# Kernel optimization log

Hardware: AMD Instinct MI355X
Metric: run time of the kernel (lower is better)

The kernel has to match this reference:

```python
import jax, jax.numpy as jnp
import numpy as np

EMBED_DIM = 1024
NUM_HEADS = 16
HEAD_DIM = EMBED_DIM // NUM_HEADS


def setup_inputs() -> dict:
    key = jax.random.key(0)
    ks = jax.random.split(key, 7)
    B, S, E = 2, 2048, EMBED_DIM
    s = 1.0 / np.sqrt(E)
    return {
        "x": jax.random.normal(ks[0], (B, S, E), dtype=jnp.float32),
        "W_qkv": jax.random.uniform(ks[1], (3 * E, E), jnp.float32, -s, s),
        "b_qkv": jax.random.uniform(ks[2], (3 * E,), jnp.float32, -s, s),
        "W_proj": jax.random.uniform(ks[3], (E, E), jnp.float32, -s, s),
        "b_proj": jax.random.uniform(ks[4], (E,), jnp.float32, -s, s),
        "gamma": jnp.ones((E,), jnp.float32),
        "beta": jnp.zeros((E,), jnp.float32),
    }


def reference(x, W_qkv, b_qkv, W_proj, b_proj, gamma, beta):
    B, S, E = x.shape
    H, D = NUM_HEADS, HEAD_DIM
    residual = x
    # fused QKV projection: [B,S,3E] -> [B,S,3,H,D]
    qkv = (jnp.einsum('bse,fe->bsf', x, W_qkv) + b_qkv).reshape(B, S, 3, H, D)
    q = qkv[:, :, 0].transpose(0, 2, 1, 3)  # [B,H,S,D]
    k = qkv[:, :, 1].transpose(0, 2, 1, 3)
    v = qkv[:, :, 2].transpose(0, 2, 1, 3)
    scale = 1.0 / jnp.sqrt(jnp.float32(D)).astype(x.dtype)
    attn = jnp.einsum('bhqd,bhkd->bhqk', q, k) * scale  # [B,H,S,S]
    attn = jax.nn.softmax(attn, axis=-1)
    out = jnp.einsum('bhqk,bhkd->bhqd', attn, v)  # [B,H,S,D]
    out = out.transpose(0, 2, 1, 3).reshape(B, S, E)
    out = jnp.einsum('bse,fe->bsf', out, W_proj) + b_proj
    # LayerNorm(out + residual), eps=1e-5 (torch default)
    y = out + residual
    mu = jnp.mean(y, axis=-1, keepdims=True)
    var = jnp.mean(jnp.square(y - mu), axis=-1, keepdims=True)
    return (y - mu) * jax.lax.rsqrt(var + 1e-5) * gamma + beta
```

## Files before the change

### kernel.cpp

```cpp
#include <hip/hip_runtime.h>
#include <cstdint>

#define EDIM 1024
#define NHEADS 16
#define HDIM 64
#define BATCH 2
#define SEQ 2048
#define MROWS (BATCH * SEQ)

typedef __attribute__((ext_vector_type(8))) short bf16x8;
typedef __attribute__((ext_vector_type(4))) float f32x4;

#define QSCALE 0.18033688011112042f

__device__ __forceinline__ unsigned short f2bf(float f) {
  union { float f; unsigned u; } v; v.f = f;
  unsigned r = v.u + 0x7FFFu + ((v.u >> 16) & 1u);
  return (unsigned short)(r >> 16);
}

__device__ __forceinline__ unsigned cvt_pk_bf16(float lo, float hi) {
  unsigned r;
  asm("v_cvt_pk_bf16_f32 %0, %1, %2" : "=v"(r) : "v"(lo), "v"(hi));
  return r;
}

__device__ __forceinline__ void gload16(const void* g, void* l) {
  __builtin_amdgcn_global_load_lds(
      (const __attribute__((address_space(1))) unsigned int*)g,
      (__attribute__((address_space(3))) unsigned int*)l, 16, 0, 0);
}

__global__ __launch_bounds__(256) void cvt_all_kernel(
    const float* __restrict__ x, const float* __restrict__ wq,
    const float* __restrict__ wp, unsigned short* __restrict__ xo,
    unsigned short* __restrict__ wqo, unsigned short* __restrict__ wpo) {
  const int NX = MROWS * EDIM, NQ = 3 * EDIM * EDIM, NP = EDIM * EDIM;
  int i = (blockIdx.x * 256 + threadIdx.x) * 8;
  const float* src;
  unsigned short* dst;
  if (i < NX) {
    src = x + i; dst = xo + i;
  } else if (i < NX + NQ) {
    src = wq + (i - NX); dst = wqo + (i - NX);
  } else if (i < NX + NQ + NP) {
    src = wp + (i - NX - NQ); dst = wpo + (i - NX - NQ);
  } else {
    return;
  }
  const float4 a = *(const float4*)&src[0];
  const float4 b = *(const float4*)&src[4];
  unsigned u[4];
  u[0] = cvt_pk_bf16(a.x, a.y);
  u[1] = cvt_pk_bf16(a.z, a.w);
  u[2] = cvt_pk_bf16(b.x, b.y);
  u[3] = cvt_pk_bf16(b.z, b.w);
  *(uint4*)dst = *(uint4*)u;
}

template <int MODE>
__global__ __launch_bounds__(256) void gemm_bf16(
    const unsigned short* __restrict__ A, const unsigned short* __restrict__ Bw,
    const float* __restrict__ bias, const float* __restrict__ resid,
    unsigned short* __restrict__ q_out, unsigned short* __restrict__ k_out,
    unsigned short* __restrict__ v_out, float* __restrict__ y_out,
    int M, int N, int K) {
  __shared__ unsigned short As[128 * 64];
  __shared__ unsigned short Bs[128 * 64];
  const int tid = threadIdx.x;
  const int lane = tid & 63, w = tid >> 6;
  const int wr = w >> 1, wc = w & 1;
  const int l15 = lane & 15, g = lane >> 4;

  const int flat = blockIdx.y * gridDim.x + blockIdx.x;
  const int xk = flat & 7, xi = flat >> 3;
  int bx, by;
  if (MODE == 0) { bx = xk * 3 + (xi >> 5); by = xi & 31; }
  else           { bx = xk;                 by = xi; }
  const int row0 = by * 128, col0 = bx * 128;

  const int er = w * 32 + (lane >> 3);
  const int ec = (lane & 7) * 8;

  f32x4 acc[4][4];
#pragma unroll
  for (int i = 0; i < 4; ++i)
#pragma unroll
    for (int j = 0; j < 4; ++j) acc[i][j] = (f32x4){0.f, 0.f, 0.f, 0.f};

  for (int k0 = 0; k0 < K; k0 += 64) {
    __syncthreads();
#pragma unroll
    for (int t = 0; t < 4; ++t) {
      gload16(&A[(size_t)(row0 + er + t * 8) * K + k0 + ec],
              &As[w * 2048 + t * 512]);
      gload16(&Bw[(size_t)(col0 + er + t * 8) * K + k0 + ec],
              &Bs[w * 2048 + t * 512]);
    }
    __syncthreads();
#pragma unroll
    for (int ks = 0; ks < 2; ++ks) {
      bf16x8 af[4], bfr[4];
#pragma unroll
      for (int i = 0; i < 4; ++i)
        af[i] = *(const bf16x8*)&As[(wr * 64 + i * 16 + l15) * 64 + ks * 32 + g * 8];
#pragma unroll
      for (int j = 0; j < 4; ++j)
        bfr[j] = *(const bf16x8*)&Bs[(wc * 64 + j * 16 + l15) * 64 + ks * 32 + g * 8];
#pragma unroll
      for (int i = 0; i < 4; ++i)
#pragma unroll
        for (int j = 0; j < 4; ++j)
          acc[i][j] = __builtin_amdgcn_mfma_f32_16x16x32_bf16(af[i], bfr[j],
                                                              acc[i][j], 0, 0, 0);
    }
  }

#pragma unroll
  for (int j = 0; j < 4; ++j) {
    const int nbase = col0 + wc * 64 + j * 16 + l15;
    const float bb = bias[nbase];
#pragma unroll
    for (int i = 0; i < 4; ++i) {
#pragma unroll
      for (int r = 0; r < 4; ++r) {
        const int m = row0 + wr * 64 + i * 16 + g * 4 + r;
        float v = acc[i][j][r] + bb;
        if (MODE == 0) {
          const int which = nbase >> 10;
          const int h = (nbase >> 6) & 15, d = nbase & 63;
          const int b = m >> 11, s = m & 2047;
          const size_t idx = ((size_t)(b * NHEADS + h) * SEQ + s) * HDIM + d;
          if (which == 0) q_out[idx] = f2bf(v * QSCALE);
          else if (which == 1) k_out[idx] = f2bf(v);
          else v_out[idx] = f2bf(v);
        } else {
          v += resid[(size_t)m * N + nbase];
          y_out[(size_t)m * N + nbase] = v;
        }
      }
    }
  }
}

__global__ __launch_bounds__(256) void vtrans_kernel(
    const unsigned short* __restrict__ V, unsigned short* __restrict__ Vt) {
  __shared__ unsigned short T[64 * 72];
  const int tid = threadIdx.x;
  const int st = blockIdx.x, bh = blockIdx.y;
  const size_t ibase = (size_t)bh * SEQ * HDIM + (size_t)st * 64 * HDIM;
#pragma unroll
  for (int t = 0; t < 2; ++t) {
    const int chunk = t * 256 + tid;
    const int r = chunk >> 3, c8 = chunk & 7;
    const uint4 v = *(const uint4*)&V[ibase + r * 64 + c8 * 8];
    *(uint4*)&T[r * 72 + c8 * 8] = v;
  }
  __syncthreads();
  const size_t obase = (size_t)bh * HDIM * SEQ + st * 64;
#pragma unroll
  for (int t = 0; t < 2; ++t) {
    const int chunk = t * 256 + tid;
    const int d = chunk >> 3, s8 = (chunk & 7) * 8;
    unsigned short u[8];
#pragma unroll
    for (int e = 0; e < 8; ++e) u[e] = T[(s8 + e) * 72 + d];
    *(uint4*)&Vt[obase + (size_t)d * SEQ + s8] = *(uint4*)u;
  }
}

__global__ __launch_bounds__(512, 4) void attn_mfma(
    const unsigned short* __restrict__ Qb, const unsigned short* __restrict__ Kb,
    const unsigned short* __restrict__ Vt, unsigned short* __restrict__ AO) {
  __shared__ unsigned short K_lds[2][64 * 64];
  __shared__ unsigned short V_lds[2][64 * 64];
  __shared__ unsigned P32[128 * 32];
  const int tid = threadIdx.x;
  const int lane = tid & 63, w = tid >> 6;
  const int l15 = lane & 15, g = lane >> 4;
  const int qt = blockIdx.x;
  const int bh = blockIdx.y;
  const int b = bh >> 4, h = bh & 15;
  const size_t hbase = (size_t)bh * SEQ * HDIM;
  const size_t vbase = (size_t)bh * HDIM * SEQ;
  const int q = qt * 128 + w * 16 + l15;
  const int prow32 = (w * 16 + l15) * 32;

  const int sr = (w & 3) * 16 + (lane >> 3);
  const int scol = ((lane & 7) ^ (lane >> 3)) * 8;

  bf16x8 aq[2];
#pragma unroll
  for (int ks = 0; ks < 2; ++ks)
    aq[ks] = *(const bf16x8*)&Qb[hbase + (size_t)q * HDIM + ks * 32 + g * 8];

  f32x4 o[4];
#pragma unroll
  for (int jd = 0; jd < 4; ++jd) o[jd] = (f32x4){0.f, 0.f, 0.f, 0.f};
  float mi = -1e30f, li = 0.f;

#define STAGE(buf, kt_)                                                        \
  do {                                                                         \
    if (w < 4) {                                                               \
      gload16(&Kb[hbase + (size_t)((kt_) * 64 + sr) * HDIM + scol],            \
              &K_lds[buf][(w * 16) * 64]);                                     \
      gload16(&Kb[hbase + (size_t)((kt_) * 64 + sr + 8) * HDIM + scol],        \
              &K_lds[buf][(w * 16 + 8) * 64]);                                 \
    } else {                                                                   \
      gload16(&Vt[vbase + (size_t)sr * SEQ + (kt_) * 64 + scol],               \
              &V_lds[buf][((w - 4) * 16) * 64]);                               \
      gload16(&Vt[vbase + (size_t)(sr + 8) * SEQ + (kt_) * 64 + scol],         \
              &V_lds[buf][((w - 4) * 16 + 8) * 64]);                           \
    }                                                                          \
  } while (0)

  STAGE(0, 0);
  for (int kt = 0; kt < SEQ / 64; ++kt) {
    const int cur = kt & 1;
    __syncthreads();
    if (kt + 1 < SEQ / 64) STAGE(cur ^ 1, kt + 1);

    f32x4 scT[4];
#pragma unroll
    for (int j = 0; j < 4; ++j) scT[j] = (f32x4){0.f, 0.f, 0.f, 0.f};
    __builtin_amdgcn_s_setprio(1);
#pragma unroll
    for (int ks = 0; ks < 2; ++ks) {
      bf16x8 bk[4];
#pragma unroll
      for (int j = 0; j < 4; ++j)
        bk[j] = *(const bf16x8*)&K_lds[cur][(j * 16 + l15) * 64 +
                                            (((ks * 4 + g) ^ (l15 & 7)) * 8)];
#pragma unroll
      for (int j = 0; j < 4; ++j)
        scT[j] = __builtin_amdgcn_mfma_f32_16x16x32_bf16(bk[j], aq[ks],
                                                         scT[j], 0, 0, 0);
    }
    __builtin_amdgcn_s_setprio(0);

    float tm = scT[0][0];
#pragma unroll
    for (int j = 0; j < 4; ++j)
#pragma unroll
      for (int r = 0; r < 4; ++r) tm = fmaxf(tm, scT[j][r]);
    tm = fmaxf(tm, __shfl_xor(tm, 16));
    tm = fmaxf(tm, __shfl_xor(tm, 32));
    const bool defer = __all(tm <= mi + 8.f) != 0;
    float al = 1.f;
    if (!defer) {
      const float mn = fmaxf(mi, tm);
      al = exp2f(mi - mn);
      mi = mn;
#pragma unroll
      for (int jd = 0; jd < 4; ++jd)
#pragma unroll
        for (int r = 0; r < 4; ++r) o[jd][r] *= al;
    }
    float p[4][4];
    float rs = 0.f;
#pragma unroll
    for (int j = 0; j < 4; ++j)
#pragma unroll
      for (int r = 0; r < 4; ++r) {
        p[j][r] = exp2f(scT[j][r] - mi);
        rs += p[j][r];
      }
    rs += __shfl_xor(rs, 16);
    rs += __shfl_xor(rs, 32);
    li = li * al + rs;

#pragma unroll
    for (int j = 0; j < 4; ++j) {
      const unsigned u01 = cvt_pk_bf16(p[j][0], p[j][1]);
      const unsigned u23 = cvt_pk_bf16(p[j][2], p[j][3]);
      const int c = (j * 4 + g) ^ l15;
      *(uint2*)&P32[prow32 + c * 2] = make_uint2(u01, u23);
    }

    __builtin_amdgcn_s_setprio(1);
#pragma unroll
    for (int ks = 0; ks < 2; ++ks) {
      const int cb = ks * 8 + g * 2;
      const uint2 a0 = *(const uint2*)&P32[prow32 + ((cb) ^ l15) * 2];
      const uint2 a1 = *(const uint2*)&P32[prow32 + ((cb + 1) ^ l15) * 2];
      unsigned pa[4] = {a0.x, a0.y, a1.x, a1.y};
      const bf16x8 ap = *(const bf16x8*)pa;
      bf16x8 bv[4];
#pragma unroll
      for (int jd = 0; jd < 4; ++jd)
        bv[jd] = *(const bf16x8*)&V_lds[cur][(jd * 16 + l15) * 64 +
                                             (((ks * 4 + g) ^ (l15 & 7)) * 8)];
#pragma unroll
      for (int jd = 0; jd < 4; ++jd)
        o[jd] = __builtin_amdgcn_mfma_f32_16x16x32_bf16(bv[jd], ap, o[jd], 0, 0, 0);
    }
    __builtin_amdgcn_s_setprio(0);
  }
#undef STAGE

  const float inv = 1.f / li;
#pragma unroll
  for (int jd = 0; jd < 4; ++jd) {
    uint2 u;
    u.x = cvt_pk_bf16(o[jd][0] * inv, o[jd][1] * inv);
    u.y = cvt_pk_bf16(o[jd][2] * inv, o[jd][3] * inv);
    *(uint2*)&AO[(size_t)(b * SEQ + q) * EDIM + h * HDIM + jd * 16 + g * 4] = u;
  }
}

__global__ __launch_bounds__(256) void ln_kernel(float* __restrict__ y,
                                                 const float* __restrict__ gamma,
                                                 const float* __restrict__ beta) {
  const int row = blockIdx.x, tid = threadIdx.x;
  const float4 v = *reinterpret_cast<const float4*>(&y[(size_t)row * EDIM + tid * 4]);
  float s = v.x + v.y + v.z + v.w;
  float s2 = v.x * v.x + v.y * v.y + v.z * v.z + v.w * v.w;
#pragma unroll
  for (int off = 1; off < 64; off <<= 1) {
    s += __shfl_xor(s, off);
    s2 += __shfl_xor(s2, off);
  }
  __shared__ float red[8];
  if ((tid & 63) == 0) {
    red[(tid >> 6) * 2 + 0] = s;
    red[(tid >> 6) * 2 + 1] = s2;
  }
  __syncthreads();
  s = red[0] + red[2] + red[4] + red[6];
  s2 = red[1] + red[3] + red[5] + red[7];
  const float mean = s * (1.f / 1024.f);
  const float var = fmaxf(s2 * (1.f / 1024.f) - mean * mean, 0.f);
  const float rstd = rsqrtf(var + 1e-5f);
  const float4 gm = *reinterpret_cast<const float4*>(&gamma[tid * 4]);
  const float4 be = *reinterpret_cast<const float4*>(&beta[tid * 4]);
  float4 outv;
  outv.x = (v.x - mean) * rstd * gm.x + be.x;
  outv.y = (v.y - mean) * rstd * gm.y + be.y;
  outv.z = (v.z - mean) * rstd * gm.z + be.z;
  outv.w = (v.w - mean) * rstd * gm.w + be.w;
  *reinterpret_cast<float4*>(&y[(size_t)row * EDIM + tid * 4]) = outv;
}

extern "C" void kernel_launch(void* const* d_in, const int* in_sizes, int n_in,
                              void* d_out, int out_size, void* d_ws,
                              size_t ws_size, hipStream_t stream) {
  const float* x = (const float*)d_in[0];
  const float* W_qkv = (const float*)d_in[1];
  const float* b_qkv = (const float*)d_in[2];
  const float* W_proj = (const float*)d_in[3];
  const float* b_proj = (const float*)d_in[4];
  const float* gamma = (const float*)d_in[5];
  const float* beta = (const float*)d_in[6];
  float* out = (float*)d_out;

  uint8_t* p = (uint8_t*)d_ws;
  unsigned short* x_bf = (unsigned short*)p;            p += (size_t)MROWS * EDIM * 2;
  unsigned short* wqkv_bf = (unsigned short*)p;         p += (size_t)3 * EDIM * EDIM * 2;
  unsigned short* wproj_bf = (unsigned short*)p;        p += (size_t)EDIM * EDIM * 2;
  unsigned short* Qb = (unsigned short*)p;              p += (size_t)MROWS * EDIM * 2;
  unsigned short* Kb = (unsigned short*)p;              p += (size_t)MROWS * EDIM * 2;
  unsigned short* Vb = (unsigned short*)p;              p += (size_t)MROWS * EDIM * 2;
  unsigned short* Vtb = (unsigned short*)p;             p += (size_t)MROWS * EDIM * 2;
  unsigned short* AOb = (unsigned short*)p;             p += (size_t)MROWS * EDIM * 2;

  const int NCVT = MROWS * EDIM + 3 * EDIM * EDIM + EDIM * EDIM;
  cvt_all_kernel<<<(NCVT / 8 + 255) / 256, 256, 0, stream>>>(
      x, W_qkv, W_proj, x_bf, wqkv_bf, wproj_bf);

  gemm_bf16<0><<<dim3(24, 32), 256, 0, stream>>>(x_bf, wqkv_bf, b_qkv, nullptr,
                                                 Qb, Kb, Vb, nullptr,
                                                 MROWS, 3 * EDIM, EDIM);
  vtrans_kernel<<<dim3(SEQ / 64, BATCH * NHEADS), 256, 0, stream>>>(Vb, Vtb);
  attn_mfma<<<dim3(SEQ / 128, BATCH * NHEADS), 512, 0, stream>>>(Qb, Kb, Vtb, AOb);
  gemm_bf16<1><<<dim3(8, 32), 256, 0, stream>>>(AOb, wproj_bf, b_proj, x,
                                                nullptr, nullptr, nullptr, out,
                                                MROWS, EDIM, EDIM);
  ln_kernel<<<MROWS, 256, 0, stream>>>(out, gamma, beta);
}
```

Before: 248.3 us.

## Halve proj GEMM row tile, remap attention grid, compute softmax row sums via MFMA

After: 245.4 us. About the same (-1.2%).

```diff
diff --git a/kernel.cpp b/kernel.cpp
--- a/kernel.cpp
+++ b/kernel.cpp
@@ -65,7 +65,9 @@
     unsigned short* __restrict__ q_out, unsigned short* __restrict__ k_out,
     unsigned short* __restrict__ v_out, float* __restrict__ y_out,
     int M, int N, int K) {
-  __shared__ unsigned short As[128 * 64];
+  constexpr int BM = (MODE == 0) ? 128 : 64;
+  constexpr int IR = BM / 32;
+  __shared__ unsigned short As[BM * 64];
   __shared__ unsigned short Bs[128 * 64];
   const int tid = threadIdx.x;
   const int lane = tid & 63, w = tid >> 6;
@@ -77,38 +79,41 @@
   int bx, by;
   if (MODE == 0) { bx = xk * 3 + (xi >> 5); by = xi & 31; }
   else           { bx = xk;                 by = xi; }
-  const int row0 = by * 128, col0 = bx * 128;
-
-  const int er = w * 32 + (lane >> 3);
+  const int row0 = by * BM, col0 = bx * 128;
+
+  const int erA = w * (BM / 4) + (lane >> 3);
+  const int erB = w * 32 + (lane >> 3);
   const int ec = (lane & 7) * 8;
 
-  f32x4 acc[4][4];
-#pragma unroll
-  for (int i = 0; i < 4; ++i)
+  f32x4 acc[IR][4];
+#pragma unroll
+  for (int i = 0; i < IR; ++i)
 #pragma unroll
     for (int j = 0; j < 4; ++j) acc[i][j] = (f32x4){0.f, 0.f, 0.f, 0.f};
 
   for (int k0 = 0; k0 < K; k0 += 64) {
     __syncthreads();
 #pragma unroll
-    for (int t = 0; t < 4; ++t) {
-      gload16(&A[(size_t)(row0 + er + t * 8) * K + k0 + ec],
-              &As[w * 2048 + t * 512]);
-      gload16(&Bw[(size_t)(col0 + er + t * 8) * K + k0 + ec],
+    for (int t = 0; t < BM / 32; ++t)
+      gload16(&A[(size_t)(row0 + erA + t * 8) * K + k0 + ec],
+              &As[w * (BM * 16) + t * 512]);
+#pragma unroll
+    for (int t = 0; t < 4; ++t)
+      gload16(&Bw[(size_t)(col0 + erB + t * 8) * K + k0 + ec],
               &Bs[w * 2048 + t * 512]);
-    }
     __syncthreads();
 #pragma unroll
     for (int ks = 0; ks < 2; ++ks) {
-      bf16x8 af[4], bfr[4];
-#pragma unroll
-      for (int i = 0; i < 4; ++i)
-        af[i] = *(const bf16x8*)&As[(wr * 64 + i * 16 + l15) * 64 + ks * 32 + g * 8];
+      bf16x8 af[IR], bfr[4];
+#pragma unroll
+      for (int i = 0; i < IR; ++i)
+        af[i] = *(const bf16x8*)&As[(wr * (BM / 2) + i * 16 + l15) * 64 +
+                                    ks * 32 + g * 8];
 #pragma unroll
       for (int j = 0; j < 4; ++j)
         bfr[j] = *(const bf16x8*)&Bs[(wc * 64 + j * 16 + l15) * 64 + ks * 32 + g * 8];
 #pragma unroll
-      for (int i = 0; i < 4; ++i)
+      for (int i = 0; i < IR; ++i)
 #pragma unroll
         for (int j = 0; j < 4; ++j)
           acc[i][j] = __builtin_amdgcn_mfma_f32_16x16x32_bf16(af[i], bfr[j],
@@ -121,10 +126,10 @@
     const int nbase = col0 + wc * 64 + j * 16 + l15;
     const float bb = bias[nbase];
 #pragma unroll
-    for (int i = 0; i < 4; ++i) {
+    for (int i = 0; i < IR; ++i) {
 #pragma unroll
       for (int r = 0; r < 4; ++r) {
-        const int m = row0 + wr * 64 + i * 16 + g * 4 + r;
+        const int m = row0 + wr * (BM / 2) + i * 16 + g * 4 + r;
         float v = acc[i][j][r] + bb;
         if (MODE == 0) {
           const int which = nbase >> 10;
@@ -174,17 +179,19 @@
     const unsigned short* __restrict__ Vt, unsigned short* __restrict__ AO) {
   __shared__ unsigned short K_lds[2][64 * 64];
   __shared__ unsigned short V_lds[2][64 * 64];
-  __shared__ unsigned P32[128 * 32];
+  __shared__ unsigned short P_lds[128 * 80];
   const int tid = threadIdx.x;
   const int lane = tid & 63, w = tid >> 6;
   const int l15 = lane & 15, g = lane >> 4;
-  const int qt = blockIdx.x;
-  const int bh = blockIdx.y;
+  const int flat = blockIdx.y * gridDim.x + blockIdx.x;
+  const int xk = flat & 7, xi = flat >> 3;
+  const int qt = xi & 15;
+  const int bh = xk * 4 + (xi >> 4);
   const int b = bh >> 4, h = bh & 15;
   const size_t hbase = (size_t)bh * SEQ * HDIM;
   const size_t vbase = (size_t)bh * HDIM * SEQ;
   const int q = qt * 128 + w * 16 + l15;
-  const int prow32 = (w * 16 + l15) * 32;
+  const int prow = (w * 16 + l15) * 80;
 
   const int sr = (w & 3) * 16 + (lane >> 3);
   const int scol = ((lane & 7) ^ (lane >> 3)) * 8;
@@ -194,10 +201,15 @@
   for (int ks = 0; ks < 2; ++ks)
     aq[ks] = *(const bf16x8*)&Qb[hbase + (size_t)q * HDIM + ks * 32 + g * 8];
 
+  unsigned short ones_s[8] = {0x3F80, 0x3F80, 0x3F80, 0x3F80,
+                              0x3F80, 0x3F80, 0x3F80, 0x3F80};
+  const bf16x8 ones8 = *(const bf16x8*)ones_s;
+
   f32x4 o[4];
 #pragma unroll
   for (int jd = 0; jd < 4; ++jd) o[jd] = (f32x4){0.f, 0.f, 0.f, 0.f};
-  float mi = -1e30f, li = 0.f;
+  f32x4 lacc = (f32x4){0.f, 0.f, 0.f, 0.f};
+  float mi = -1e30f;
 
 #define STAGE(buf, kt_)                                                        \
   do {                                                                         \
@@ -238,53 +250,37 @@
     }
     __builtin_amdgcn_s_setprio(0);
 
-    float tm = scT[0][0];
-#pragma unroll
-    for (int j = 0; j < 4; ++j)
-#pragma unroll
-      for (int r = 0; r < 4; ++r) tm = fmaxf(tm, scT[j][r]);
+    const float m0 = fmaxf(fmaxf(scT[0][0], scT[0][1]), scT[0][2]);
+    const float m1 = fmaxf(fmaxf(scT[0][3], scT[1][0]), scT[1][1]);
+    const float m2 = fmaxf(fmaxf(scT[1][2], scT[1][3]), scT[2][0]);
+    const float m3 = fmaxf(fmaxf(scT[2][1], scT[2][2]), scT[2][3]);
+    const float m4 = fmaxf(fmaxf(scT[3][0], scT[3][1]), scT[3][2]);
+    float tm = fmaxf(fmaxf(fmaxf(m0, m1), m2),
+                     fmaxf(fmaxf(m3, m4), scT[3][3]));
     tm = fmaxf(tm, __shfl_xor(tm, 16));
     tm = fmaxf(tm, __shfl_xor(tm, 32));
-    const bool defer = __all(tm <= mi + 8.f) != 0;
-    float al = 1.f;
-    if (!defer) {
-      const float mn = fmaxf(mi, tm);
-      al = exp2f(mi - mn);
-      mi = mn;
-#pragma unroll
-      for (int jd = 0; jd < 4; ++jd)
-#pragma unroll
-        for (int r = 0; r < 4; ++r) o[jd][r] *= al;
-    }
-    float p[4][4];
-    float rs = 0.f;
-#pragma unroll
-    for (int j = 0; j < 4; ++j)
-#pragma unroll
-      for (int r = 0; r < 4; ++r) {
-        p[j][r] = exp2f(scT[j][r] - mi);
-        rs += p[j][r];
-      }
-    rs += __shfl_xor(rs, 16);
-    rs += __shfl_xor(rs, 32);
-    li = li * al + rs;
-
+    const float mn = fmaxf(mi, tm);
+    const float al = exp2f(mi - mn);
+    mi = mn;
+#pragma unroll
+    for (int jd = 0; jd < 4; ++jd)
+#pragma unroll
+      for (int r = 0; r < 4; ++r) o[jd][r] *= al;
+    lacc[0] *= al;
 #pragma unroll
     for (int j = 0; j < 4; ++j) {
-      const unsigned u01 = cvt_pk_bf16(p[j][0], p[j][1]);
-      const unsigned u23 = cvt_pk_bf16(p[j][2], p[j][3]);
-      const int c = (j * 4 + g) ^ l15;
-      *(uint2*)&P32[prow32 + c * 2] = make_uint2(u01, u23);
+      const float p0 = exp2f(scT[j][0] - mi);
+      const float p1 = exp2f(scT[j][1] - mi);
+      const float p2 = exp2f(scT[j][2] - mi);
+      const float p3 = exp2f(scT[j][3] - mi);
+      *(unsigned*)&P_lds[prow + j * 16 + g * 4 + 0] = cvt_pk_bf16(p0, p1);
+      *(unsigned*)&P_lds[prow + j * 16 + g * 4 + 2] = cvt_pk_bf16(p2, p3);
     }
 
     __builtin_amdgcn_s_setprio(1);
 #pragma unroll
     for (int ks = 0; ks < 2; ++ks) {
-      const int cb = ks * 8 + g * 2;
-      const uint2 a0 = *(const uint2*)&P32[prow32 + ((cb) ^ l15) * 2];
-      const uint2 a1 = *(const uint2*)&P32[prow32 + ((cb + 1) ^ l15) * 2];
-      unsigned pa[4] = {a0.x, a0.y, a1.x, a1.y};
-      const bf16x8 ap = *(const bf16x8*)pa;
+      const bf16x8 ap = *(const bf16x8*)&P_lds[prow + ks * 32 + g * 8];
       bf16x8 bv[4];
 #pragma unroll
       for (int jd = 0; jd < 4; ++jd)
@@ -293,12 +289,13 @@
 #pragma unroll
       for (int jd = 0; jd < 4; ++jd)
         o[jd] = __builtin_amdgcn_mfma_f32_16x16x32_bf16(bv[jd], ap, o[jd], 0, 0, 0);
+      lacc = __builtin_amdgcn_mfma_f32_16x16x32_bf16(ones8, ap, lacc, 0, 0, 0);
     }
     __builtin_amdgcn_s_setprio(0);
   }
 #undef STAGE
 
-  const float inv = 1.f / li;
+  const float inv = 1.f / lacc[0];
 #pragma unroll
   for (int jd = 0; jd < 4; ++jd) {
     uint2 u;
@@ -372,7 +369,7 @@
                                                  MROWS, 3 * EDIM, EDIM);
   vtrans_kernel<<<dim3(SEQ / 64, BATCH * NHEADS), 256, 0, stream>>>(Vb, Vtb);
   attn_mfma<<<dim3(SEQ / 128, BATCH * NHEADS), 512, 0, stream>>>(Qb, Kb, Vtb, AOb);
-  gemm_bf16<1><<<dim3(8, 32), 256, 0, stream>>>(AOb, wproj_bf, b_proj, x,
+  gemm_bf16<1><<<dim3(8, 64), 256, 0, stream>>>(AOb, wproj_bf, b_proj, x,
                                                 nullptr, nullptr, nullptr, out,
                                                 MROWS, EDIM, EDIM);
   ln_kernel<<<MROWS, 256, 0, stream>>>(out, gamma, beta);
```
